# Performance work log

Hardware: AMD Instinct MI355X
Metric: run time of the kernel (lower is better)

## Reference

```python
import jax, jax.numpy as jnp
import numpy as np

N = 100000   # nodes
E = 1600000  # edges (avg degree 16)
F_IN = 128   # num_features
H = 128      # num_hidden
C = 40       # num_classes


def setup_inputs() -> dict:
    key = jax.random.key(0)
    ks = jax.random.split(key, 8)
    w = lambda k, sh: jax.random.normal(k, sh, dtype=jnp.float32) * 0.05
    return {
        "x": jax.random.normal(ks[0], (N, F_IN), dtype=jnp.float32),
        "edge_index": jax.random.randint(ks[1], (2, E), 0, N),
        "W_rel1": w(ks[2], (F_IN, H)),
        "b_rel1": jnp.zeros((H,), jnp.float32),
        "W_root1": w(ks[3], (F_IN, H)),
        "W_rel2": w(ks[4], (H, H)),
        "b_rel2": jnp.zeros((H,), jnp.float32),
        "W_root2": w(ks[5], (H, H)),
        "W_lin": w(ks[6], (2 * H, C)),
        "b_lin": jnp.zeros((C,), jnp.float32),
    }


def _graph_conv(x, src, dst, W_rel, b_rel, W_root, n):
    # PyG GraphConv: sum_{j in N(i)} x_j -> lin_rel, plus lin_root(x_i)
    agg = jax.ops.segment_sum(x[src], dst, num_segments=n)  # [N, d_in]
    return agg @ W_rel + b_rel + x @ W_root


def reference(x, edge_index, W_rel1, b_rel1, W_root1, W_rel2, b_rel2, W_root2, W_lin, b_lin):
    src, dst = edge_index[0], edge_index[1]
    n = x.shape[0]
    # dropout is identity at inference (training=False)
    x1 = jax.nn.relu(_graph_conv(x, src, dst, W_rel1, b_rel1, W_root1, n))
    x2 = jax.nn.relu(_graph_conv(x1, src, dst, W_rel2, b_rel2, W_root2, n))
    h = jnp.concatenate([x1, x2], axis=-1)  # [N, 2H]
    return jax.nn.log_softmax(h @ W_lin + b_lin, axis=-1)
```

## Files before the change

### kernel.cpp

```cpp
#include <hip/hip_runtime.h>
#include <hip/hip_bf16.h>

typedef __attribute__((ext_vector_type(8))) short bf16x8;
typedef __attribute__((ext_vector_type(4))) float f32x4;

#define EPB 4096
#define BUCKET_BITS 10
#define BUCKET_SIZE 1024

static __device__ __forceinline__ unsigned short f2bf(float f) {
    union { float f; unsigned u; } v; v.f = f;
    unsigned r = v.u + 0x7FFF + ((v.u >> 16) & 1);
    return (unsigned short)(r >> 16);
}
static __device__ __forceinline__ float bf2f(unsigned short h) {
    union { unsigned u; float f; } v; v.u = ((unsigned)h) << 16;
    return v.f;
}

__global__ __launch_bounds__(256) void cvt_bf16(const float* __restrict__ x,
                                                unsigned short* __restrict__ out, int n4) {
    int i = blockIdx.x * 256 + threadIdx.x;
    if (i >= n4) return;
    float4 v = ((const float4*)x)[i];
    ushort4 o;
    o.x = f2bf(v.x); o.y = f2bf(v.y); o.z = f2bf(v.z); o.w = f2bf(v.w);
    ((ushort4*)out)[i] = o;
}

__global__ __launch_bounds__(256) void build_bsw(const float* __restrict__ Wrel,
                                                 const float* __restrict__ Wroot,
                                                 unsigned short* __restrict__ bsw) {
    int idx = blockIdx.x * 256 + threadIdx.x;
    int j = idx & 7, L = (idx >> 3) & 63, ct = (idx >> 9) & 15, kt = idx >> 13;
    int k = kt * 32 + ((L >> 4) * 8) + j;
    int c = ct * 16 + (L & 15);
    float v = (c < 128) ? Wrel[k * 128 + c] : Wroot[k * 128 + (c - 128)];
    bsw[idx] = f2bf(v);
}

__global__ __launch_bounds__(256) void build_bswL(const float* __restrict__ Wlin,
                                                  unsigned short* __restrict__ bsw, int total) {
    int idx = blockIdx.x * 256 + threadIdx.x;
    if (idx >= total) return;
    int t = idx;
    int j = t & 7; t >>= 3;
    int L = t & 63; t >>= 6;
    int ct = t % 3;
    int kt = t / 3;
    int k = kt * 32 + ((L >> 4) * 8) + j;
    int c = ct * 16 + (L & 15);
    float v = (c < 40) ? Wlin[k * 40 + c] : 0.f;
    bsw[idx] = f2bf(v);
}


__global__ __launch_bounds__(256) void edge_hist(const int* __restrict__ dst,
                                                 int* __restrict__ hist,
                                                 int E, int nblk, int nbuck) {
    __shared__ int h[128];
    int t = threadIdx.x, blk = blockIdx.x;
    if (t < nbuck) h[t] = 0;
    __syncthreads();
    int e0 = blk * EPB;
#pragma unroll
    for (int it = 0; it < EPB / 256; it++) {
        int e = e0 + it * 256 + t;
        if (e < E) atomicAdd(&h[dst[e] >> BUCKET_BITS], 1);
    }
    __syncthreads();
    if (t < nbuck) hist[t * nblk + blk] = h[t];
}

__global__ __launch_bounds__(256) void bucket_total(const int* __restrict__ hist,
                                                    int* __restrict__ total, int nblk) {
    __shared__ int s[256];
    int b = blockIdx.x, t = threadIdx.x;
    int v = 0;
    for (int i = t; i < nblk; i += 256) v += hist[b * nblk + i];
    s[t] = v; __syncthreads();
#pragma unroll
    for (int o = 128; o >= 1; o >>= 1) {
        if (t < o) s[t] += s[t + o];
        __syncthreads();
    }
    if (t == 0) total[b] = s[0];
}

__global__ __launch_bounds__(128) void bucket_scan(const int* __restrict__ total,
                                                   int* __restrict__ base, int nbuck) {
    __shared__ int s[128];
    int t = threadIdx.x;
    int v = (t < nbuck) ? total[t] : 0;
    s[t] = v; __syncthreads();
#pragma unroll
    for (int o = 1; o < 128; o <<= 1) {
        int x = (t >= o) ? s[t - o] : 0;
        __syncthreads();
        s[t] += x; __syncthreads();
    }
    if (t < nbuck) base[t] = s[t] - v;
    if (t == 127) base[nbuck] = s[127];
}

__global__ __launch_bounds__(256) void block_scan(int* __restrict__ hist,
                                                  const int* __restrict__ base, int nblk) {
    __shared__ int s[256];
    __shared__ int carry;
    int b = blockIdx.x, t = threadIdx.x;
    if (t == 0) carry = base[b];
    __syncthreads();
    for (int start = 0; start < nblk; start += 256) {
        int i = start + t;
        int v = (i < nblk) ? hist[b * nblk + i] : 0;
        s[t] = v; __syncthreads();
#pragma unroll
        for (int o = 1; o < 256; o <<= 1) {
            int x = (t >= o) ? s[t - o] : 0;
            __syncthreads();
            s[t] += x; __syncthreads();
        }
        int excl = s[t] - v + carry;
        if (i < nblk) hist[b * nblk + i] = excl;
        if (t == 255) carry += s[255];
        __syncthreads();
    }
}

__global__ __launch_bounds__(256) void edge_part(const int* __restrict__ src,
                                                 const int* __restrict__ dst,
                                                 const int* __restrict__ hist,
                                                 int* __restrict__ part,
                                                 int E, int nblk, int nbuck) {
    __shared__ int hcnt[128];
    __shared__ int lstart[128];
    __shared__ int cur[128];
    __shared__ int gbase[128];
    __shared__ int ssc[128];
    __shared__ int sdst[EPB];
    __shared__ int ssrc[EPB];
    int t = threadIdx.x, blk = blockIdx.x;
    int e0 = blk * EPB;
    int cnt = E - e0; if (cnt > EPB) cnt = EPB;
    if (t < nbuck) { hcnt[t] = 0; gbase[t] = hist[t * nblk + blk]; }
    __syncthreads();
    int myd[EPB / 256], mys[EPB / 256];
#pragma unroll
    for (int it = 0; it < EPB / 256; it++) {
        int i = it * 256 + t;
        if (i < cnt) {
            myd[it] = dst[e0 + i];
            mys[it] = src[e0 + i];
            atomicAdd(&hcnt[myd[it] >> BUCKET_BITS], 1);
        }
    }
    __syncthreads();
    if (t < 128) ssc[t] = (t < nbuck) ? hcnt[t] : 0;
    __syncthreads();
#pragma unroll
    for (int o = 1; o < 128; o <<= 1) {
        int x = 0;
        if (t < 128 && t >= o) x = ssc[t - o];
        __syncthreads();
        if (t < 128) ssc[t] += x;
        __syncthreads();
    }
    if (t < nbuck) { lstart[t] = ssc[t] - hcnt[t]; cur[t] = 0; }
    __syncthreads();
#pragma unroll
    for (int it = 0; it < EPB / 256; it++) {
        int i = it * 256 + t;
        if (i < cnt) {
            int b = myd[it] >> BUCKET_BITS;
            int p = lstart[b] + atomicAdd(&cur[b], 1);
            sdst[p] = myd[it];
            ssrc[p] = mys[it];
        }
    }
    __syncthreads();
    for (int i = t; i < cnt; i += 256) {
        int d = sdst[i], s = ssrc[i];
        int b = d >> BUCKET_BITS;
        part[gbase[b] + (i - lstart[b])] = ((d & (BUCKET_SIZE - 1)) << 17) | s;
    }
}

__global__ __launch_bounds__(256) void csr_finalize(const int* __restrict__ part,
                                                    const int* __restrict__ bucketBase,
                                                    int* __restrict__ off_,
                                                    int* __restrict__ deg_,
                                                    int* __restrict__ csr_src,
                                                    int N) {
    __shared__ int cur[BUCKET_SIZE];
    __shared__ int h[BUCKET_SIZE];
    __shared__ int tsum[256];
    int b = blockIdx.x, t = threadIdx.x;
    int lo = bucketBase[b], hi = bucketBase[b + 1];
    int n0 = b * BUCKET_SIZE;
    for (int i = t; i < BUCKET_SIZE; i += 256) h[i] = 0;
    __syncthreads();
    for (int i = lo + t; i < hi; i += 256) atomicAdd(&h[part[i] >> 17], 1);
    __syncthreads();
    int a0 = h[4 * t], a1 = h[4 * t + 1], a2 = h[4 * t + 2], a3 = h[4 * t + 3];
    int ts = a0 + a1 + a2 + a3;
    tsum[t] = ts;
    __syncthreads();
#pragma unroll
    for (int o = 1; o < 256; o <<= 1) {
        int x = (t >= o) ? tsum[t - o] : 0;
        __syncthreads();
        tsum[t] += x;
        __syncthreads();
    }
    int st0 = tsum[t] - ts;
    int st1 = st0 + a0, st2 = st1 + a1, st3 = st2 + a2;
    cur[4 * t] = st0; cur[4 * t + 1] = st1; cur[4 * t + 2] = st2; cur[4 * t + 3] = st3;
    int node = n0 + 4 * t;
    if (node < N)     { off_[node] = lo + st0;     deg_[node] = a0; }
    if (node + 1 < N) { off_[node + 1] = lo + st1; deg_[node + 1] = a1; }
    if (node + 2 < N) { off_[node + 2] = lo + st2; deg_[node + 2] = a2; }
    if (node + 3 < N) { off_[node + 3] = lo + st3; deg_[node + 3] = a3; }
    __syncthreads();
    for (int i = lo + t; i < hi; i += 256) {
        int rec = part[i];
        int p = atomicAdd(&cur[rec >> 17], 1);
        csr_src[lo + p] = rec & 0x1FFFF;
    }
}

__global__ __launch_bounds__(256) void gemm_layer(const unsigned short* __restrict__ Abf,
                                                  const unsigned short* __restrict__ Bsw,
                                                  const float* __restrict__ bias,
                                                  unsigned short* __restrict__ xr,
                                                  float* __restrict__ accbuf, int N) {
    int wid = blockIdx.x * 4 + (threadIdx.x >> 6);
    int L = threadIdx.x & 63;
    int r0 = wid * 16;
    if (r0 >= N) return;
    int arow = r0 + (L & 15);
    const bf16x8* Aptr = (const bf16x8*)(Abf + (size_t)arow * 128 + ((L >> 4) * 8));
    const bf16x8* Bptr = ((const bf16x8*)Bsw) + L;
    f32x4 acc[16];
#pragma unroll
    for (int i = 0; i < 16; i++) acc[i] = (f32x4){0.f, 0.f, 0.f, 0.f};
#pragma unroll
    for (int kt = 0; kt < 4; kt++) {
        bf16x8 a = Aptr[kt * 4];
#pragma unroll
        for (int ct = 0; ct < 16; ct++) {
            bf16x8 b = Bptr[(kt * 16 + ct) * 64];
            acc[ct] = __builtin_amdgcn_mfma_f32_16x16x32_bf16(a, b, acc[ct], 0, 0, 0);
        }
    }
    int rbase = r0 + (L >> 4) * 4;
    int cl = L & 15;
#pragma unroll
    for (int ct = 0; ct < 16; ct++) {
        int col = ct * 16 + cl;
#pragma unroll
        for (int r = 0; r < 4; r++) {
            int row = rbase + r;
            float v = acc[ct][r];
            if (col < 128)
                xr[(size_t)row * 128 + col] = f2bf(v);
            else
                accbuf[(size_t)row * 128 + (col - 128)] = v + bias[col - 128];
        }
    }
}

__global__ __launch_bounds__(256) void agg_relu_cvt(const unsigned short* __restrict__ xr,
                                                    const float* __restrict__ acc,
                                                    const int* __restrict__ off_,
                                                    const int* __restrict__ deg,
                                                    const int* __restrict__ csr_src,
                                                    unsigned short* __restrict__ out, int N) {
    int node = blockIdx.x * 4 + (threadIdx.x >> 6);
    if (node >= N) return;
    int L = threadIdx.x & 63;
    int g = L >> 4;
    int f = L & 15;
    int o = off_[node];
    int d = deg[node];
    float af[8];
#pragma unroll
    for (int i = 0; i < 8; i++) af[i] = 0.f;

    for (int k = 0; k < d; k += 64) {
        int chunk = (d - k < 64) ? (d - k) : 64;
        int id = (L < chunk) ? csr_src[o + k + L] : 0;
        int full = chunk & ~3;
#pragma unroll 4
        for (int j = 0; j < full; j += 4) {
            int s = __shfl(id, j + g, 64);
            bf16x8 p = *(const bf16x8*)(xr + (size_t)s * 128 + f * 8);
#pragma unroll
            for (int i = 0; i < 8; i++) af[i] += bf2f((unsigned short)p[i]);
        }
        if (full < chunk) {
            int sl = full + g;
            int s = __shfl(id, (sl < chunk) ? sl : 0, 64);
            if (sl < chunk) {
                bf16x8 p = *(const bf16x8*)(xr + (size_t)s * 128 + f * 8);
#pragma unroll
                for (int i = 0; i < 8; i++) af[i] += bf2f((unsigned short)p[i]);
            }
        }
    }
#pragma unroll
    for (int i = 0; i < 8; i++) af[i] += __shfl_xor(af[i], 16, 64);
#pragma unroll
    for (int i = 0; i < 8; i++) af[i] += __shfl_xor(af[i], 32, 64);

    if (g == 0) {
        const float* ap = acc + (size_t)node * 128 + f * 8;
        float4 a0 = *(const float4*)ap;
        float4 a1 = *(const float4*)(ap + 4);
        float r0 = fmaxf(a0.x + af[0], 0.f), r1 = fmaxf(a0.y + af[1], 0.f);
        float r2 = fmaxf(a0.z + af[2], 0.f), r3 = fmaxf(a0.w + af[3], 0.f);
        float r4 = fmaxf(a1.x + af[4], 0.f), r5 = fmaxf(a1.y + af[5], 0.f);
        float r6 = fmaxf(a1.z + af[6], 0.f), r7 = fmaxf(a1.w + af[7], 0.f);
        uint4 wv;
        wv.x = ((unsigned)f2bf(r1) << 16) | f2bf(r0);
        wv.y = ((unsigned)f2bf(r3) << 16) | f2bf(r2);
        wv.z = ((unsigned)f2bf(r5) << 16) | f2bf(r4);
        wv.w = ((unsigned)f2bf(r7) << 16) | f2bf(r6);
        *(uint4*)(out + (size_t)node * 128 + f * 8) = wv;
    }
}

__global__ __launch_bounds__(256) void gemm_final(const unsigned short* __restrict__ x1bf,
                                                  const unsigned short* __restrict__ x2bf,
                                                  const unsigned short* __restrict__ Bsw,
                                                  const float* __restrict__ blin,
                                                  float* __restrict__ logits, int N) {
    int wid = blockIdx.x * 4 + (threadIdx.x >> 6);
    int L = threadIdx.x & 63;
    int r0 = wid * 16;
    if (r0 >= N) return;
    int arow = r0 + (L & 15);
    f32x4 acc[3];
#pragma unroll
    for (int i = 0; i < 3; i++) acc[i] = (f32x4){0.f, 0.f, 0.f, 0.f};
#pragma unroll
    for (int kt = 0; kt < 8; kt++) {
        const unsigned short* Ab = (kt < 4) ? x1bf : x2bf;
        int kk = (kt & 3) * 32 + ((L >> 4) * 8);
        bf16x8 a = *((const bf16x8*)(Ab + (size_t)arow * 128 + kk));
#pragma unroll
        for (int ct = 0; ct < 3; ct++) {
            bf16x8 b = ((const bf16x8*)Bsw)[(kt * 3 + ct) * 64 + L];
            acc[ct] = __builtin_amdgcn_mfma_f32_16x16x32_bf16(a, b, acc[ct], 0, 0, 0);
        }
    }
    int rbase = r0 + (L >> 4) * 4;
    int cl = L & 15;
#pragma unroll
    for (int ct = 0; ct < 3; ct++) {
        int col = ct * 16 + cl;
        if (col < 40) {
#pragma unroll
            for (int r = 0; r < 4; r++) {
                logits[(size_t)(rbase + r) * 40 + col] = acc[ct][r] + blin[col];
            }
        }
    }
}

__global__ __launch_bounds__(256) void log_softmax_k(const float* __restrict__ logits,
                                                     float* __restrict__ out, int N) {
    int node = blockIdx.x * 4 + (threadIdx.x >> 6);
    if (node >= N) return;
    int L = threadIdx.x & 63;
    float v = (L < 40) ? logits[(size_t)node * 40 + L] : -__builtin_inff();
    float m = v;
#pragma unroll
    for (int off = 32; off >= 1; off >>= 1) m = fmaxf(m, __shfl_xor(m, off, 64));
    float e = (L < 40) ? __expf(v - m) : 0.f;
    float s = e;
#pragma unroll
    for (int off = 32; off >= 1; off >>= 1) s += __shfl_xor(s, off, 64);
    if (L < 40) out[(size_t)node * 40 + L] = v - m - __logf(s);
}

extern "C" void kernel_launch(void* const* d_in, const int* in_sizes, int n_in,
                              void* d_out, int out_size, void* d_ws, size_t ws_size,
                              hipStream_t stream) {
    const float* x      = (const float*)d_in[0];
    const int*   edge   = (const int*)d_in[1];
    const float* Wrel1  = (const float*)d_in[2];
    const float* brel1  = (const float*)d_in[3];
    const float* Wroot1 = (const float*)d_in[4];
    const float* Wrel2  = (const float*)d_in[5];
    const float* brel2  = (const float*)d_in[6];
    const float* Wroot2 = (const float*)d_in[7];
    const float* Wlin   = (const float*)d_in[8];
    const float* blin   = (const float*)d_in[9];

    const int N = in_sizes[0] / 128;
    const int E = in_sizes[1] / 2;
    const int* src = edge;
    const int* dst = edge + E;

    const int nblk  = (E + EPB - 1) / EPB;
    const int nbuck = (N + BUCKET_SIZE - 1) / BUCKET_SIZE;

    char* ws = (char*)d_ws;
    size_t off = 0;
    auto alloc = [&](size_t bytes) -> void* {
        void* p = ws + off;
        off += (bytes + 255) & ~(size_t)255;
        return p;
    };
    unsigned short* xbf  = (unsigned short*)alloc((size_t)N * 128 * 2);
    unsigned short* x1bf = (unsigned short*)alloc((size_t)N * 128 * 2);
    unsigned short* xr   = (unsigned short*)alloc((size_t)N * 128 * 2);
    float* acc1          = (float*)alloc((size_t)N * 128 * 4);
    float* acc2          = (float*)alloc((size_t)N * 128 * 4);
    unsigned short* bsw1 = (unsigned short*)alloc(32768 * 2);
    unsigned short* bsw2 = (unsigned short*)alloc(32768 * 2);
    unsigned short* bswL = (unsigned short*)alloc(12288 * 2);
    int* hist       = (int*)alloc((size_t)nbuck * nblk * 4);
    int* bucketTot  = (int*)alloc((size_t)nbuck * 4);
    int* bucketBase = (int*)alloc((size_t)(nbuck + 1) * 4);
    int* part       = (int*)alloc((size_t)E * 4);
    int* csr_src    = (int*)alloc((size_t)E * 4);
    int* off_       = (int*)alloc((size_t)N * 4);
    int* deg_       = (int*)alloc((size_t)N * 4);
    unsigned short* x2bf = xbf;
    float* logits        = acc1;

    const int n4 = (N * 128) / 4;
    const int cvtBlocks = (n4 + 255) / 256;
    const int rowTiles = (N + 15) / 16;
    const int gemmBlocks = (rowTiles + 3) / 4;
    const int nodeBlocks = (N + 3) / 4;

    build_bsw<<<128, 256, 0, stream>>>(Wrel1, Wroot1, bsw1);
    build_bsw<<<128, 256, 0, stream>>>(Wrel2, Wroot2, bsw2);
    build_bswL<<<48, 256, 0, stream>>>(Wlin, bswL, 12288);
    cvt_bf16<<<cvtBlocks, 256, 0, stream>>>(x, xbf, n4);

    edge_hist<<<nblk, 256, 0, stream>>>(dst, hist, E, nblk, nbuck);
    bucket_total<<<nbuck, 256, 0, stream>>>(hist, bucketTot, nblk);
    bucket_scan<<<1, 128, 0, stream>>>(bucketTot, bucketBase, nbuck);
    block_scan<<<nbuck, 256, 0, stream>>>(hist, bucketBase, nblk);
    edge_part<<<nblk, 256, 0, stream>>>(src, dst, hist, part, E, nblk, nbuck);
    csr_finalize<<<nbuck, 256, 0, stream>>>(part, bucketBase, off_, deg_, csr_src, N);

    gemm_layer<<<gemmBlocks, 256, 0, stream>>>(xbf, bsw1, brel1, xr, acc1, N);
    agg_relu_cvt<<<nodeBlocks, 256, 0, stream>>>(xr, acc1, off_, deg_, csr_src, x1bf, N);

    gemm_layer<<<gemmBlocks, 256, 0, stream>>>(x1bf, bsw2, brel2, xr, acc2, N);
    agg_relu_cvt<<<nodeBlocks, 256, 0, stream>>>(xr, acc2, off_, deg_, csr_src, x2bf, N);

    gemm_final<<<gemmBlocks, 256, 0, stream>>>(x1bf, x2bf, bswL, blin, logits, N);
    log_softmax_k<<<nodeBlocks, 256, 0, stream>>>(logits, (float*)d_out, N);
}
```

Measured before the change: 410.7 us.

## Fuse prep kernels, scans, x conversion and log-softmax; store root accumulator as bf16

Weight swizzles and the edge histogram now run in one kernel, and the three scan kernels collapse into one. The fp32-to-bf16 conversion of x moves into the first GEMM's A load, and log-softmax moves into the final GEMM epilogue. The root-term accumulator is stored as bf16 instead of fp32. Together these cut launch count and global memory traffic. In exchange, every scan_all block redundantly re-reduces the whole histogram, and rounding the root term to bf16 adds precision loss.

```diff
diff --git a/kernel.cpp b/kernel.cpp
--- a/kernel.cpp
+++ b/kernel.cpp
@@ -18,98 +18,83 @@
     return v.f;
 }
 
-__global__ __launch_bounds__(256) void cvt_bf16(const float* __restrict__ x,
-                                                unsigned short* __restrict__ out, int n4) {
-    int i = blockIdx.x * 256 + threadIdx.x;
-    if (i >= n4) return;
-    float4 v = ((const float4*)x)[i];
-    ushort4 o;
-    o.x = f2bf(v.x); o.y = f2bf(v.y); o.z = f2bf(v.z); o.w = f2bf(v.w);
-    ((ushort4*)out)[i] = o;
-}
-
-__global__ __launch_bounds__(256) void build_bsw(const float* __restrict__ Wrel,
-                                                 const float* __restrict__ Wroot,
-                                                 unsigned short* __restrict__ bsw) {
-    int idx = blockIdx.x * 256 + threadIdx.x;
-    int j = idx & 7, L = (idx >> 3) & 63, ct = (idx >> 9) & 15, kt = idx >> 13;
-    int k = kt * 32 + ((L >> 4) * 8) + j;
-    int c = ct * 16 + (L & 15);
-    float v = (c < 128) ? Wrel[k * 128 + c] : Wroot[k * 128 + (c - 128)];
-    bsw[idx] = f2bf(v);
-}
-
-__global__ __launch_bounds__(256) void build_bswL(const float* __restrict__ Wlin,
-                                                  unsigned short* __restrict__ bsw, int total) {
-    int idx = blockIdx.x * 256 + threadIdx.x;
-    if (idx >= total) return;
-    int t = idx;
-    int j = t & 7; t >>= 3;
-    int L = t & 63; t >>= 6;
-    int ct = t % 3;
-    int kt = t / 3;
-    int k = kt * 32 + ((L >> 4) * 8) + j;
-    int c = ct * 16 + (L & 15);
-    float v = (c < 40) ? Wlin[k * 40 + c] : 0.f;
-    bsw[idx] = f2bf(v);
-}
-
-
-__global__ __launch_bounds__(256) void edge_hist(const int* __restrict__ dst,
-                                                 int* __restrict__ hist,
-                                                 int E, int nblk, int nbuck) {
+__global__ __launch_bounds__(256) void prep(const float* __restrict__ Wrel1,
+                                            const float* __restrict__ Wroot1,
+                                            const float* __restrict__ Wrel2,
+                                            const float* __restrict__ Wroot2,
+                                            const float* __restrict__ Wlin,
+                                            const int* __restrict__ dst,
+                                            unsigned short* __restrict__ bsw1,
+                                            unsigned short* __restrict__ bsw2,
+                                            unsigned short* __restrict__ bswL,
+                                            int* __restrict__ hist,
+                                            int E, int nblk, int nbuck) {
     __shared__ int h[128];
-    int t = threadIdx.x, blk = blockIdx.x;
-    if (t < nbuck) h[t] = 0;
-    __syncthreads();
-    int e0 = blk * EPB;
-#pragma unroll
-    for (int it = 0; it < EPB / 256; it++) {
-        int e = e0 + it * 256 + t;
-        if (e < E) atomicAdd(&h[dst[e] >> BUCKET_BITS], 1);
-    }
-    __syncthreads();
-    if (t < nbuck) hist[t * nblk + blk] = h[t];
-}
-
-__global__ __launch_bounds__(256) void bucket_total(const int* __restrict__ hist,
-                                                    int* __restrict__ total, int nblk) {
+    int blk = blockIdx.x, t = threadIdx.x;
+    if (blk < 256) {
+        const float* Wrel  = (blk < 128) ? Wrel1 : Wrel2;
+        const float* Wroot = (blk < 128) ? Wroot1 : Wroot2;
+        unsigned short* bsw = (blk < 128) ? bsw1 : bsw2;
+        int idx = (blk & 127) * 256 + t;
+        int j = idx & 7, L = (idx >> 3) & 63, ct = (idx >> 9) & 15, kt = idx >> 13;
+        int k = kt * 32 + ((L >> 4) * 8) + j;
+        int c = ct * 16 + (L & 15);
+        float v = (c < 128) ? Wrel[k * 128 + c] : Wroot[k * 128 + (c - 128)];
+        bsw[idx] = f2bf(v);
+    } else if (blk < 304) {
+        int idx = (blk - 256) * 256 + t;
+        int tt = idx;
+        int j = tt & 7; tt >>= 3;
+        int L = tt & 63; tt >>= 6;
+        int ct = tt % 3;
+        int kt = tt / 3;
+        int k = kt * 32 + ((L >> 4) * 8) + j;
+        int c = ct * 16 + (L & 15);
+        float v = (c < 40) ? Wlin[k * 40 + c] : 0.f;
+        bswL[idx] = f2bf(v);
+    } else {
+        int hb = blk - 304;
+        if (t < nbuck) h[t] = 0;
+        __syncthreads();
+        int e0 = hb * EPB;
+#pragma unroll
+        for (int it = 0; it < EPB / 256; it++) {
+            int e = e0 + it * 256 + t;
+            if (e < E) atomicAdd(&h[dst[e] >> BUCKET_BITS], 1);
+        }
+        __syncthreads();
+        if (t < nbuck) hist[t * nblk + hb] = h[t];
+    }
+}
+
+__global__ __launch_bounds__(256) void scan_all(int* __restrict__ hist,
+                                                int* __restrict__ bucketBase,
+                                                int nblk, int nbuck) {
+    __shared__ int tot[128];
     __shared__ int s[256];
     int b = blockIdx.x, t = threadIdx.x;
-    int v = 0;
-    for (int i = t; i < nblk; i += 256) v += hist[b * nblk + i];
-    s[t] = v; __syncthreads();
-#pragma unroll
-    for (int o = 128; o >= 1; o >>= 1) {
-        if (t < o) s[t] += s[t + o];
-        __syncthreads();
-    }
-    if (t == 0) total[b] = s[0];
-}
-
-__global__ __launch_bounds__(128) void bucket_scan(const int* __restrict__ total,
-                                                   int* __restrict__ base, int nbuck) {
-    __shared__ int s[128];
-    int t = threadIdx.x;
-    int v = (t < nbuck) ? total[t] : 0;
-    s[t] = v; __syncthreads();
+    if (t < 128) tot[t] = 0;
+    __syncthreads();
+    int len = nbuck * nblk;
+    for (int i = t; i < len; i += 256) atomicAdd(&tot[i / nblk], hist[i]);
+    __syncthreads();
+    if (t < 128) s[t] = tot[t];
+    __syncthreads();
 #pragma unroll
     for (int o = 1; o < 128; o <<= 1) {
-        int x = (t >= o) ? s[t - o] : 0;
-        __syncthreads();
-        s[t] += x; __syncthreads();
-    }
-    if (t < nbuck) base[t] = s[t] - v;
-    if (t == 127) base[nbuck] = s[127];
-}
-
-__global__ __launch_bounds__(256) void block_scan(int* __restrict__ hist,
-                                                  const int* __restrict__ base, int nblk) {
-    __shared__ int s[256];
-    __shared__ int carry;
-    int b = blockIdx.x, t = threadIdx.x;
-    if (t == 0) carry = base[b];
-    __syncthreads();
+        int x = (t < 128 && t >= o) ? s[t - o] : 0;
+        __syncthreads();
+        if (t < 128) s[t] += x;
+        __syncthreads();
+    }
+    int base_b = s[b] - tot[b];
+    int tot_b = tot[b];
+    if (t == 0) {
+        bucketBase[b] = base_b;
+        if (b == nbuck - 1) bucketBase[nbuck] = base_b + tot_b;
+    }
+    __syncthreads();
+    int carryv = base_b;
     for (int start = 0; start < nblk; start += 256) {
         int i = start + t;
         int v = (i < nblk) ? hist[b * nblk + i] : 0;
@@ -120,9 +105,9 @@
             __syncthreads();
             s[t] += x; __syncthreads();
         }
-        int excl = s[t] - v + carry;
+        int excl = s[t] - v + carryv;
         if (i < nblk) hist[b * nblk + i] = excl;
-        if (t == 255) carry += s[255];
+        carryv += s[255];
         __syncthreads();
     }
 }
@@ -228,24 +213,35 @@
     }
 }
 
-__global__ __launch_bounds__(256) void gemm_layer(const unsigned short* __restrict__ Abf,
-                                                  const unsigned short* __restrict__ Bsw,
-                                                  const float* __restrict__ bias,
-                                                  unsigned short* __restrict__ xr,
-                                                  float* __restrict__ accbuf, int N) {
+template <bool AF32>
+__global__ __launch_bounds__(256) void gemm_layer_t(const void* __restrict__ A,
+                                                    const unsigned short* __restrict__ Bsw,
+                                                    const float* __restrict__ bias,
+                                                    unsigned short* __restrict__ xr,
+                                                    unsigned short* __restrict__ accbf, int N) {
     int wid = blockIdx.x * 4 + (threadIdx.x >> 6);
     int L = threadIdx.x & 63;
     int r0 = wid * 16;
     if (r0 >= N) return;
     int arow = r0 + (L & 15);
-    const bf16x8* Aptr = (const bf16x8*)(Abf + (size_t)arow * 128 + ((L >> 4) * 8));
     const bf16x8* Bptr = ((const bf16x8*)Bsw) + L;
     f32x4 acc[16];
 #pragma unroll
     for (int i = 0; i < 16; i++) acc[i] = (f32x4){0.f, 0.f, 0.f, 0.f};
 #pragma unroll
     for (int kt = 0; kt < 4; kt++) {
-        bf16x8 a = Aptr[kt * 4];
+        bf16x8 a;
+        if (AF32) {
+            const float* Arow = ((const float*)A) + (size_t)arow * 128 + ((L >> 4) * 8) + kt * 32;
+            float4 a0 = *(const float4*)Arow;
+            float4 a1 = *(const float4*)(Arow + 4);
+            a[0] = (short)f2bf(a0.x); a[1] = (short)f2bf(a0.y);
+            a[2] = (short)f2bf(a0.z); a[3] = (short)f2bf(a0.w);
+            a[4] = (short)f2bf(a1.x); a[5] = (short)f2bf(a1.y);
+            a[6] = (short)f2bf(a1.z); a[7] = (short)f2bf(a1.w);
+        } else {
+            a = *((const bf16x8*)(((const unsigned short*)A) + (size_t)arow * 128 + ((L >> 4) * 8) + kt * 32));
+        }
 #pragma unroll
         for (int ct = 0; ct < 16; ct++) {
             bf16x8 b = Bptr[(kt * 16 + ct) * 64];
@@ -264,13 +260,13 @@
             if (col < 128)
                 xr[(size_t)row * 128 + col] = f2bf(v);
             else
-                accbuf[(size_t)row * 128 + (col - 128)] = v + bias[col - 128];
+                accbf[(size_t)row * 128 + (col - 128)] = f2bf(v + bias[col - 128]);
         }
     }
 }
 
 __global__ __launch_bounds__(256) void agg_relu_cvt(const unsigned short* __restrict__ xr,
-                                                    const float* __restrict__ acc,
+                                                    const unsigned short* __restrict__ accbf,
                                                     const int* __restrict__ off_,
                                                     const int* __restrict__ deg,
                                                     const int* __restrict__ csr_src,
@@ -313,27 +309,30 @@
     for (int i = 0; i < 8; i++) af[i] += __shfl_xor(af[i], 32, 64);
 
     if (g == 0) {
-        const float* ap = acc + (size_t)node * 128 + f * 8;
-        float4 a0 = *(const float4*)ap;
-        float4 a1 = *(const float4*)(ap + 4);
-        float r0 = fmaxf(a0.x + af[0], 0.f), r1 = fmaxf(a0.y + af[1], 0.f);
-        float r2 = fmaxf(a0.z + af[2], 0.f), r3 = fmaxf(a0.w + af[3], 0.f);
-        float r4 = fmaxf(a1.x + af[4], 0.f), r5 = fmaxf(a1.y + af[5], 0.f);
-        float r6 = fmaxf(a1.z + af[6], 0.f), r7 = fmaxf(a1.w + af[7], 0.f);
+        bf16x8 a = *(const bf16x8*)(accbf + (size_t)node * 128 + f * 8);
         uint4 wv;
-        wv.x = ((unsigned)f2bf(r1) << 16) | f2bf(r0);
-        wv.y = ((unsigned)f2bf(r3) << 16) | f2bf(r2);
-        wv.z = ((unsigned)f2bf(r5) << 16) | f2bf(r4);
-        wv.w = ((unsigned)f2bf(r7) << 16) | f2bf(r6);
+        unsigned short rlo, rhi;
+        rlo = f2bf(fmaxf(bf2f((unsigned short)a[0]) + af[0], 0.f));
+        rhi = f2bf(fmaxf(bf2f((unsigned short)a[1]) + af[1], 0.f));
+        wv.x = ((unsigned)rhi << 16) | rlo;
+        rlo = f2bf(fmaxf(bf2f((unsigned short)a[2]) + af[2], 0.f));
+        rhi = f2bf(fmaxf(bf2f((unsigned short)a[3]) + af[3], 0.f));
+        wv.y = ((unsigned)rhi << 16) | rlo;
+        rlo = f2bf(fmaxf(bf2f((unsigned short)a[4]) + af[4], 0.f));
+        rhi = f2bf(fmaxf(bf2f((unsigned short)a[5]) + af[5], 0.f));
+        wv.z = ((unsigned)rhi << 16) | rlo;
+        rlo = f2bf(fmaxf(bf2f((unsigned short)a[6]) + af[6], 0.f));
+        rhi = f2bf(fmaxf(bf2f((unsigned short)a[7]) + af[7], 0.f));
+        wv.w = ((unsigned)rhi << 16) | rlo;
         *(uint4*)(out + (size_t)node * 128 + f * 8) = wv;
     }
 }
 
-__global__ __launch_bounds__(256) void gemm_final(const unsigned short* __restrict__ x1bf,
-                                                  const unsigned short* __restrict__ x2bf,
-                                                  const unsigned short* __restrict__ Bsw,
-                                                  const float* __restrict__ blin,
-                                                  float* __restrict__ logits, int N) {
+__global__ __launch_bounds__(256) void gemm_final_ls(const unsigned short* __restrict__ x1bf,
+                                                     const unsigned short* __restrict__ x2bf,
+                                                     const unsigned short* __restrict__ Bsw,
+                                                     const float* __restrict__ blin,
+                                                     float* __restrict__ out, int N) {
     int wid = blockIdx.x * 4 + (threadIdx.x >> 6);
     int L = threadIdx.x & 63;
     int r0 = wid * 16;
@@ -355,32 +354,26 @@
     }
     int rbase = r0 + (L >> 4) * 4;
     int cl = L & 15;
-#pragma unroll
-    for (int ct = 0; ct < 3; ct++) {
-        int col = ct * 16 + cl;
-        if (col < 40) {
-#pragma unroll
-            for (int r = 0; r < 4; r++) {
-                logits[(size_t)(rbase + r) * 40 + col] = acc[ct][r] + blin[col];
-            }
-        }
-    }
-}
-
-__global__ __launch_bounds__(256) void log_softmax_k(const float* __restrict__ logits,
-                                                     float* __restrict__ out, int N) {
-    int node = blockIdx.x * 4 + (threadIdx.x >> 6);
-    if (node >= N) return;
-    int L = threadIdx.x & 63;
-    float v = (L < 40) ? logits[(size_t)node * 40 + L] : -__builtin_inff();
-    float m = v;
-#pragma unroll
-    for (int off = 32; off >= 1; off >>= 1) m = fmaxf(m, __shfl_xor(m, off, 64));
-    float e = (L < 40) ? __expf(v - m) : 0.f;
-    float s = e;
-#pragma unroll
-    for (int off = 32; off >= 1; off >>= 1) s += __shfl_xor(s, off, 64);
-    if (L < 40) out[(size_t)node * 40 + L] = v - m - __logf(s);
+    float b0 = blin[cl], b1 = blin[16 + cl];
+    float b2 = (cl < 8) ? blin[32 + cl] : 0.f;
+#pragma unroll
+    for (int r = 0; r < 4; r++) {
+        int row = rbase + r;
+        float v0 = acc[0][r] + b0;
+        float v1 = acc[1][r] + b1;
+        float v2 = (cl < 8) ? (acc[2][r] + b2) : -__builtin_inff();
+        float m = fmaxf(fmaxf(v0, v1), v2);
+#pragma unroll
+        for (int off = 8; off >= 1; off >>= 1) m = fmaxf(m, __shfl_xor(m, off, 64));
+        float e = __expf(v0 - m) + __expf(v1 - m) + ((cl < 8) ? __expf(v2 - m) : 0.f);
+#pragma unroll
+        for (int off = 8; off >= 1; off >>= 1) e += __shfl_xor(e, off, 64);
+        float ls = m + __logf(e);
+        float* op = out + (size_t)row * 40;
+        op[cl] = v0 - ls;
+        op[16 + cl] = v1 - ls;
+        if (cl < 8) op[32 + cl] = v2 - ls;
+    }
 }
 
 extern "C" void kernel_launch(void* const* d_in, const int* in_sizes, int n_in,
@@ -412,48 +405,35 @@
         off += (bytes + 255) & ~(size_t)255;
         return p;
     };
-    unsigned short* xbf  = (unsigned short*)alloc((size_t)N * 128 * 2);
     unsigned short* x1bf = (unsigned short*)alloc((size_t)N * 128 * 2);
+    unsigned short* x2bf = (unsigned short*)alloc((size_t)N * 128 * 2);
     unsigned short* xr   = (unsigned short*)alloc((size_t)N * 128 * 2);
-    float* acc1          = (float*)alloc((size_t)N * 128 * 4);
-    float* acc2          = (float*)alloc((size_t)N * 128 * 4);
+    unsigned short* accbf= (unsigned short*)alloc((size_t)N * 128 * 2);
     unsigned short* bsw1 = (unsigned short*)alloc(32768 * 2);
     unsigned short* bsw2 = (unsigned short*)alloc(32768 * 2);
     unsigned short* bswL = (unsigned short*)alloc(12288 * 2);
     int* hist       = (int*)alloc((size_t)nbuck * nblk * 4);
-    int* bucketTot  = (int*)alloc((size_t)nbuck * 4);
     int* bucketBase = (int*)alloc((size_t)(nbuck + 1) * 4);
     int* part       = (int*)alloc((size_t)E * 4);
     int* csr_src    = (int*)alloc((size_t)E * 4);
     int* off_       = (int*)alloc((size_t)N * 4);
     int* deg_       = (int*)alloc((size_t)N * 4);
-    unsigned short* x2bf = xbf;
-    float* logits        = acc1;
-
-    const int n4 = (N * 128) / 4;
-    const int cvtBlocks = (n4 + 255) / 256;
+
     const int rowTiles = (N + 15) / 16;
     const int gemmBlocks = (rowTiles + 3) / 4;
     const int nodeBlocks = (N + 3) / 4;
 
-    build_bsw<<<128, 256, 0, stream>>>(Wrel1, Wroot1, bsw1);
-    build_bsw<<<128, 256, 0, stream>>>(Wrel2, Wroot2, bsw2);
-    build_bswL<<<48, 256, 0, stream>>>(Wlin, bswL, 12288);
-    cvt_bf16<<<cvtBlocks, 256, 0, stream>>>(x, xbf, n4);
-
-    edge_hist<<<nblk, 256, 0, stream>>>(dst, hist, E, nblk, nbuck);
-    bucket_total<<<nbuck, 256, 0, stream>>>(hist, bucketTot, nblk);
-    bucket_scan<<<1, 128, 0, stream>>>(bucketTot, bucketBase, nbuck);
-    block_scan<<<nbuck, 256, 0, stream>>>(hist, bucketBase, nblk);
+    prep<<<304 + nblk, 256, 0, stream>>>(Wrel1, Wroot1, Wrel2, Wroot2, Wlin, dst,
+                                         bsw1, bsw2, bswL, hist, E, nblk, nbuck);
+    scan_all<<<nbuck, 256, 0, stream>>>(hist, bucketBase, nblk, nbuck);
     edge_part<<<nblk, 256, 0, stream>>>(src, dst, hist, part, E, nblk, nbuck);
     csr_finalize<<<nbuck, 256, 0, stream>>>(part, bucketBase, off_, deg_, csr_src, N);
 
-    gemm_layer<<<gemmBlocks, 256, 0, stream>>>(xbf, bsw1, brel1, xr, acc1, N);
-    agg_relu_cvt<<<nodeBlocks, 256, 0, stream>>>(xr, acc1, off_, deg_, csr_src, x1bf, N);
-
-    gemm_layer<<<gemmBlocks, 256, 0, stream>>>(x1bf, bsw2, brel2, xr, acc2, N);
-    agg_relu_cvt<<<nodeBlocks, 256, 0, stream>>>(xr, acc2, off_, deg_, csr_src, x2bf, N);
-
-    gemm_final<<<gemmBlocks, 256, 0, stream>>>(x1bf, x2bf, bswL, blin, logits, N);
-    log_softmax_k<<<nodeBlocks, 256, 0, stream>>>(logits, (float*)d_out, N);
-}
+    gemm_layer_t<true><<<gemmBlocks, 256, 0, stream>>>(x, bsw1, brel1, xr, accbf, N);
+    agg_relu_cvt<<<nodeBlocks, 256, 0, stream>>>(xr, accbf, off_, deg_, csr_src, x1bf, N);
+
+    gemm_layer_t<false><<<gemmBlocks, 256, 0, stream>>>(x1bf, bsw2, brel2, xr, accbf, N);
+    agg_relu_cvt<<<nodeBlocks, 256, 0, stream>>>(xr, accbf, off_, deg_, csr_src, x2bf, N);
+
+    gemm_final_ls<<<gemmBlocks, 256, 0, stream>>>(x1bf, x2bf, bswL, blin, (float*)d_out, N);
+}
```

After: 408.0 us. About the same (-0.7%).
